# Kernel tuning notes

Hardware: AMD Instinct MI355X
Metric: run time of the kernel (lower is better)

The kernel has to match this reference:

```python
import jax, jax.numpy as jnp
import numpy as np


def _params_to_tokens(params):
    # (batch, 2k) -> (batch, k, 2) : chunk into freqs/amps then stack
    freqs, amps = jnp.split(params, 2, axis=-1)
    return jnp.stack((freqs, amps), axis=-1)


def setup_inputs() -> dict:
    key = jax.random.key(0)
    k1, k2 = jax.random.split(key)
    predicted = jax.random.normal(k1, (64, 4096), dtype=jnp.float32)
    target = jax.random.normal(k2, (64, 4096), dtype=jnp.float32)
    return {"predicted": predicted, "target": target}


def reference(predicted, target):
    p = _params_to_tokens(predicted)   # (b, k, 2)
    t = _params_to_tokens(target)      # (b, k, 2)
    # Euclidean cdist via gram-matrix identity (avoids (b,k,k,2) broadcast temp)
    p2 = jnp.sum(p * p, axis=-1)       # (b, k)
    t2 = jnp.sum(t * t, axis=-1)       # (b, k)
    gram = jnp.einsum('bid,bjd->bij', p, t)  # (b, k, k)
    sq = p2[:, :, None] + t2[:, None, :] - 2.0 * gram
    costs = jnp.sqrt(jnp.maximum(sq, 0.0))   # (b, k, k)
    min1 = jnp.mean(jnp.min(costs, axis=1), axis=-1)  # min over predicted dim
    min2 = jnp.mean(jnp.min(costs, axis=2), axis=-1)  # min over target dim
    return jnp.mean(min1 + min2)
```

## Files before the change

kernel.cpp:

```cpp
#include <hip/hip_runtime.h>


typedef float v2f __attribute__((ext_vector_type(2)));

constexpr int K = 2048;
constexpr int BLOCK = 1024;
constexpr int Q = 16;
constexpr int NW = BLOCK / 64;
constexpr int WJ = K / NW;
constexpr unsigned INF_U = 0x7F800000u;

__global__ __launch_bounds__(BLOCK, 4) void chamfer_kernel(
    const float* __restrict__ pred, const float* __restrict__ targ,
    float* __restrict__ out) {
  const int qhalf = blockIdx.x;
  const int b     = blockIdx.y;
  const int dir   = blockIdx.z;

  const float* qbase = (dir == 0 ? pred : targ) + (size_t)b * (2 * K);
  const float* obase = (dir == 0 ? targ : pred) + (size_t)b * (2 * K);

  const int tid  = threadIdx.x;
  const int lane = tid & 63;
  const int w    = tid >> 6;

  __shared__ float4   smem4[K / 2];
  __shared__ unsigned rowmin_u[BLOCK];
  __shared__ float    wsum[NW];

  {
    const float2* o2 = (const float2*)obase;
    const float2 xx = o2[tid];
    const float2 yy = o2[(K / 2) + tid];
    smem4[tid] = make_float4(xx.x, xx.y, yy.x, yy.y);
    rowmin_u[tid] = INF_U;
  }

  float nx[Q], ny[Q], p2[Q], mins[Q];
  #pragma unroll
  for (int q = 0; q < Q; ++q) {
    const int qi = qhalf * (64 * Q) + q * 64 + lane;
    const float px = qbase[qi];
    const float py = qbase[K + qi];
    nx[q]   = -2.0f * px;
    ny[q]   = -2.0f * py;
    p2[q]   = fmaf(px, px, py * py);
    mins[q] = 3.4e38f;
  }
  __syncthreads();

  const float4* sbase = smem4 + w * (WJ / 2);
  #pragma unroll 4
  for (int j2 = 0; j2 < WJ / 2; ++j2) {
    const float4 a = sbase[j2];
    v2f xs; xs.x = a.x; xs.y = a.y;
    v2f ys; ys.x = a.z; ys.y = a.w;
    const v2f t2 = __builtin_elementwise_fma(ys, ys, xs * xs);
    #pragma unroll
    for (int q = 0; q < Q; ++q) {
      const v2f nxq = {nx[q], nx[q]};
      const v2f nyq = {ny[q], ny[q]};
      const v2f s = __builtin_elementwise_fma(
          nyq, ys, __builtin_elementwise_fma(nxq, xs, t2));
      mins[q] = fminf(fminf(s.x, s.y), mins[q]);
    }
  }

  #pragma unroll
  for (int q = 0; q < Q; ++q) {
    const float cand = fmaxf(mins[q] + p2[q], 0.0f);
    atomicMin(&rowmin_u[q * 64 + lane], __float_as_uint(cand));
  }
  __syncthreads();

  float v = sqrtf(__uint_as_float(rowmin_u[tid]));
  #pragma unroll
  for (int off = 32; off; off >>= 1) v += __shfl_down(v, off, 64);
  if (lane == 0) wsum[w] = v;
  __syncthreads();
  if (w == 0) {
    float s = (lane < NW) ? wsum[lane] : 0.0f;
    #pragma unroll
    for (int off = 8; off; off >>= 1) s += __shfl_down(s, off, 64);
    if (lane == 0) atomicAdd(out, s * (1.0f / 131072.0f));
  }
}

extern "C" void kernel_launch(void* const* d_in, const int* in_sizes, int n_in,
                              void* d_out, int out_size, void* d_ws, size_t ws_size,
                              hipStream_t stream) {
  const float* pred = (const float*)d_in[0];
  const float* targ = (const float*)d_in[1];
  float* out = (float*)d_out;

  dim3 grid(2, 64, 2);
  chamfer_kernel<<<grid, dim3(BLOCK), 0, stream>>>(pred, targ, out);
}
```

Before: 88.20 us.

## Split work into smaller blocks with 2D query/target partitioning per block

Replaces the 1024-thread blocks (16 queries per thread, 16 waves splitting the targets) with 256-thread blocks. Each 32-thread group now owns 8 queries, and 8 groups split the target range. The grid grows fourfold to 1024 blocks. The goal is better load balance, lower per-thread register pressure and better latency hiding through more, smaller blocks. The cost is that every block reloads the full target set into shared memory, and the per-target t2 term is shared across only 8 queries instead of 16.

```diff
diff --git a/kernel.cpp b/kernel.cpp
--- a/kernel.cpp
+++ b/kernel.cpp
@@ -4,85 +4,89 @@
 typedef float v2f __attribute__((ext_vector_type(2)));
 
 constexpr int K = 2048;
-constexpr int BLOCK = 1024;
-constexpr int Q = 16;
-constexpr int NW = BLOCK / 64;
-constexpr int WJ = K / NW;
+constexpr int BLOCK = 256;
+constexpr int Q = 8;
+constexpr int S = 8;
+constexpr int QT = 32;
+constexpr int JT = K / S;
 constexpr unsigned INF_U = 0x7F800000u;
 
 __global__ __launch_bounds__(BLOCK, 4) void chamfer_kernel(
     const float* __restrict__ pred, const float* __restrict__ targ,
     float* __restrict__ out) {
-  const int qhalf = blockIdx.x;
-  const int b     = blockIdx.y;
-  const int dir   = blockIdx.z;
+  const int tile = blockIdx.x;
+  const int b    = blockIdx.y;
+  const int dir  = blockIdx.z;
 
   const float* qbase = (dir == 0 ? pred : targ) + (size_t)b * (2 * K);
   const float* obase = (dir == 0 ? targ : pred) + (size_t)b * (2 * K);
 
-  const int tid  = threadIdx.x;
-  const int lane = tid & 63;
-  const int w    = tid >> 6;
+  const int tid = threadIdx.x;
+  const int t   = tid & (QT - 1);
+  const int s   = tid >> 5;
 
   __shared__ float4   smem4[K / 2];
   __shared__ unsigned rowmin_u[BLOCK];
-  __shared__ float    wsum[NW];
+  __shared__ float    wsum[BLOCK / 64];
 
   {
     const float2* o2 = (const float2*)obase;
-    const float2 xx = o2[tid];
-    const float2 yy = o2[(K / 2) + tid];
-    smem4[tid] = make_float4(xx.x, xx.y, yy.x, yy.y);
+    #pragma unroll
+    for (int i = tid; i < K / 2; i += BLOCK) {
+      const float2 xx = o2[i];
+      const float2 yy = o2[(K / 2) + i];
+      smem4[i] = make_float4(xx.x, xx.y, yy.x, yy.y);
+    }
     rowmin_u[tid] = INF_U;
   }
 
-  float nx[Q], ny[Q], p2[Q], mins[Q];
+  v2f nxv[Q], nyv[Q];
+  float p2[Q], mins[Q];
   #pragma unroll
   for (int q = 0; q < Q; ++q) {
-    const int qi = qhalf * (64 * Q) + q * 64 + lane;
+    const int qi = tile * (QT * Q) + q * QT + t;
     const float px = qbase[qi];
     const float py = qbase[K + qi];
-    nx[q]   = -2.0f * px;
-    ny[q]   = -2.0f * py;
+    nxv[q].x = -2.0f * px; nxv[q].y = -2.0f * px;
+    nyv[q].x = -2.0f * py; nyv[q].y = -2.0f * py;
     p2[q]   = fmaf(px, px, py * py);
     mins[q] = 3.4e38f;
   }
   __syncthreads();
 
-  const float4* sbase = smem4 + w * (WJ / 2);
+  const float4* sbase = smem4 + s * (JT / 2);
   #pragma unroll 4
-  for (int j2 = 0; j2 < WJ / 2; ++j2) {
+  for (int j2 = 0; j2 < JT / 2; ++j2) {
     const float4 a = sbase[j2];
     v2f xs; xs.x = a.x; xs.y = a.y;
     v2f ys; ys.x = a.z; ys.y = a.w;
     const v2f t2 = __builtin_elementwise_fma(ys, ys, xs * xs);
     #pragma unroll
     for (int q = 0; q < Q; ++q) {
-      const v2f nxq = {nx[q], nx[q]};
-      const v2f nyq = {ny[q], ny[q]};
-      const v2f s = __builtin_elementwise_fma(
-          nyq, ys, __builtin_elementwise_fma(nxq, xs, t2));
-      mins[q] = fminf(fminf(s.x, s.y), mins[q]);
+      const v2f sc = __builtin_elementwise_fma(
+          nyv[q], ys, __builtin_elementwise_fma(nxv[q], xs, t2));
+      mins[q] = fminf(fminf(sc.x, sc.y), mins[q]);
     }
   }
 
   #pragma unroll
   for (int q = 0; q < Q; ++q) {
     const float cand = fmaxf(mins[q] + p2[q], 0.0f);
-    atomicMin(&rowmin_u[q * 64 + lane], __float_as_uint(cand));
+    atomicMin(&rowmin_u[q * QT + t], __float_as_uint(cand));
   }
   __syncthreads();
 
   float v = sqrtf(__uint_as_float(rowmin_u[tid]));
   #pragma unroll
   for (int off = 32; off; off >>= 1) v += __shfl_down(v, off, 64);
+  const int lane = tid & 63, w = tid >> 6;
   if (lane == 0) wsum[w] = v;
   __syncthreads();
   if (w == 0) {
-    float s = (lane < NW) ? wsum[lane] : 0.0f;
+    float sum = (lane < BLOCK / 64) ? wsum[lane] : 0.0f;
     #pragma unroll
-    for (int off = 8; off; off >>= 1) s += __shfl_down(s, off, 64);
-    if (lane == 0) atomicAdd(out, s * (1.0f / 131072.0f));
+    for (int off = 2; off; off >>= 1) sum += __shfl_down(sum, off, 64);
+    if (lane == 0) atomicAdd(out, sum * (1.0f / 131072.0f));
   }
 }
 
@@ -93,6 +97,6 @@
   const float* targ = (const float*)d_in[1];
   float* out = (float*)d_out;
 
-  dim3 grid(2, 64, 2);
+  dim3 grid(K / (QT * Q), 64, 2);
   chamfer_kernel<<<grid, dim3(BLOCK), 0, stream>>>(pred, targ, out);
 }
```

After: 88.04 us. Within noise of the previous version (-0.2%).
